# Kernel tuning notes

Measured on AMD Instinct MI355X. Metric: run time of the kernel, lower is better.

## Reference

```python
import jax, jax.numpy as jnp
import numpy as np

B, N, D = 8, 256, 64  # batch, n_entities, feature dim


def setup_inputs() -> dict:
    key = jax.random.key(0)
    ks = jax.random.split(key, 8)
    s = 0.02
    return {
        "emb1": jax.random.normal(ks[0], (B, N, D), jnp.float32),
        "emb2": jax.random.normal(ks[1], (B, N, N, D), jnp.float32),
        "W1a": jax.random.normal(ks[2], (3 * D, 128), jnp.float32) * s,
        "b1a": jnp.zeros((128,), jnp.float32),
        "W1b": jax.random.normal(ks[3], (128, D), jnp.float32) * s,
        "b1b": jnp.zeros((D,), jnp.float32),
        "W2a": jax.random.normal(ks[4], (4 * D, 256), jnp.float32) * s,
        "b2a": jnp.zeros((256,), jnp.float32),
        "W2b": jax.random.normal(ks[5], (256, D), jnp.float32) * s,
        "b2b": jnp.zeros((D,), jnp.float32),
    }


def _mlp(x, Wa, ba, Wb, bb):
    h = jax.nn.relu(jnp.einsum("...i,io->...o", x, Wa) + ba)
    return jnp.einsum("...i,io->...o", h, Wb) + bb


def reference(emb1, emb2, W1a, b1a, W1b, b1b, W2a, b2a, W2b, b2b):
    # arity 1: reduce arity-2 embedding over second entity dim (max & min), concat
    red_max = jnp.max(emb2, axis=-2)           # [B,N,D]
    red_min = jnp.min(emb2, axis=-2)           # [B,N,D]
    cat1 = jnp.concatenate([emb1, red_max, red_min], axis=-1)  # [B,N,3D]

    # arity 2: expand arity-1 embedding along a new entity dim, concat with emb2
    exp = jnp.broadcast_to(emb1[:, :, None, :], emb2.shape)    # [B,N,N,D]
    cat2 = jnp.concatenate([exp, emb2], axis=-1)               # [B,N,N,2D]

    # permutation gather: position (i,j) gets [cat2[j,i], cat2[i,j]] along features
    perm2 = jnp.concatenate([jnp.transpose(cat2, (0, 2, 1, 3)), cat2], axis=-1)  # [B,N,N,4D]

    out1 = _mlp(cat1, W1a, b1a, W1b, b1b)    # [B,N,D]
    out2 = _mlp(perm2, W2a, b2a, W2b, b2b)   # [B,N,N,D]
    return (out1, out2)
```

## Files before the change

### kernel.cpp

```cpp
#include <hip/hip_runtime.h>
#include <hip/hip_bf16.h>

typedef __bf16 bf16x8 __attribute__((ext_vector_type(8)));
typedef float f32x4 __attribute__((ext_vector_type(4)));
typedef unsigned int u32;
typedef unsigned short u16;
typedef u32 u32x4 __attribute__((ext_vector_type(4)));
typedef u16 u16x4 __attribute__((ext_vector_type(4)));

__device__ __forceinline__ u16 f2bf(float x) {
  u32 u = __float_as_uint(x);
  return (u16)((u + 0x7FFFu + ((u >> 16) & 1u)) >> 16);
}

__device__ __forceinline__ bf16x8 ld_frag_lds(const u16* base, int byteOff) {
  u32x4 v = *(const u32x4*)((const char*)base + byteOff);
  return __builtin_bit_cast(bf16x8, v);
}

__device__ __forceinline__ bf16x8 ld_frag_glb(const u16* p) {
  u32x4 v = *(const u32x4*)p;
  return __builtin_bit_cast(bf16x8, v);
}

__global__ void prep_kernel(const float* __restrict__ W2a, const float* __restrict__ W2b,
                            u16* __restrict__ wfA, u16* __restrict__ wfB) {
  int t = blockIdx.x * 256 + threadIdx.x;
  if (t < 8192) {
    int lane = t & 63;
    int ks = (t >> 6) & 7;
    int ntg = t >> 9;
    int col = (ntg << 4) + (lane & 15);
    int kb = (ks << 5) + ((lane >> 4) << 3);
#pragma unroll
    for (int q = 0; q < 8; ++q)
      wfA[t * 8 + q] = f2bf(W2a[(kb + q) * 256 + col]);
  } else if (t < 10240) {
    int t2 = t - 8192;
    int lane = t2 & 63;
    int ks = (t2 >> 6) & 7;
    int ntg = t2 >> 9;
    int col = (ntg << 4) + (lane & 15);
    int kb = (ks << 5) + ((lane >> 4) << 3);
#pragma unroll
    for (int q = 0; q < 8; ++q)
      wfB[t2 * 8 + q] = f2bf(W2b[(kb + q) * 64 + col]);
  }
}

__global__ __launch_bounds__(256) void out1_kernel(
    const float* __restrict__ emb1, const float* __restrict__ emb2,
    const float* __restrict__ W1a, const float* __restrict__ b1a,
    const float* __restrict__ W1b, const float* __restrict__ b1b,
    float* __restrict__ out1) {
  int bi = blockIdx.x;
  int t = threadIdx.x;
  __shared__ float smax[4][64];
  __shared__ float smin[4][64];
  __shared__ float cat1[192];
  __shared__ float h[128];

  int d = t & 63, q = t >> 6;
  const float* base = emb2 + (size_t)bi * 256 * 64;
  float vmax = -INFINITY, vmin = INFINITY;
  for (int j = q; j < 256; j += 4) {
    float v = base[j * 64 + d];
    vmax = fmaxf(vmax, v);
    vmin = fminf(vmin, v);
  }
  smax[q][d] = vmax;
  smin[q][d] = vmin;
  __syncthreads();
  if (t < 64) {
    float mx = fmaxf(fmaxf(smax[0][t], smax[1][t]), fmaxf(smax[2][t], smax[3][t]));
    float mn = fminf(fminf(smin[0][t], smin[1][t]), fminf(smin[2][t], smin[3][t]));
    cat1[t] = emb1[bi * 64 + t];
    cat1[64 + t] = mx;
    cat1[128 + t] = mn;
  }
  __syncthreads();
  if (t < 128) {
    float acc = b1a[t];
    for (int k = 0; k < 192; ++k) acc += cat1[k] * W1a[k * 128 + t];
    h[t] = fmaxf(acc, 0.f);
  }
  __syncthreads();
  if (t < 64) {
    float acc = b1b[t];
    for (int k = 0; k < 128; ++k) acc += h[k] * W1b[k * 64 + t];
    out1[bi * 64 + t] = acc;
  }
}

__global__ __launch_bounds__(256, 2) void out2_kernel(
    const float* __restrict__ emb1, const float* __restrict__ emb2,
    const float* __restrict__ b2a, const float* __restrict__ b2b,
    const u16* __restrict__ wfA, const u16* __restrict__ wfB,
    float* __restrict__ out2) {
  __shared__ __align__(16) u16 Xs[64 * 256];
  __shared__ __align__(16) u16 Hs[64 * 256];

  int blk = blockIdx.x;
  int b = blk >> 10;
  int i = (blk >> 2) & 255;
  int j0 = (blk & 3) << 6;
  int t = threadIdx.x;
  int lane = t & 63;
  int w = t >> 6;
  int lr = lane & 15;
  int lg = lane >> 4;

  {
    int r = t >> 2;
    int c0 = (t & 3) << 4;
    const float* s0 = emb1 + ((b << 8) + j0 + r) * 64;
    const float* s1 = emb2 + ((((size_t)(b << 8) + j0 + r) << 8) + i) * 64;
    const float* s2 = emb1 + ((b << 8) + i) * 64;
    const float* s3 = emb2 + ((((size_t)(b << 8) + i) << 8) + (j0 + r)) * 64;
    const float* srcs[4] = {s0, s1, s2, s3};
#pragma unroll
    for (int seg = 0; seg < 4; ++seg) {
      const float* src = srcs[seg];
#pragma unroll
      for (int u = 0; u < 4; ++u) {
        int d = c0 + (u << 2);
        float4 v = *(const float4*)(src + d);
        u16x4 o = {f2bf(v.x), f2bf(v.y), f2bf(v.z), f2bf(v.w)};
        int byteOff = (r * 512 + ((seg << 6) + d) * 2) ^ ((r & 7) << 4);
        *(u16x4*)((char*)Xs + byteOff) = o;
      }
    }
  }
  __syncthreads();

  f32x4 acc1[4][4];
#pragma unroll
  for (int m = 0; m < 4; ++m)
#pragma unroll
    for (int nt = 0; nt < 4; ++nt) acc1[m][nt] = (f32x4){0.f, 0.f, 0.f, 0.f};

#pragma unroll
  for (int ks = 0; ks < 8; ++ks) {
    int kByte = (ks << 6) + (lg << 4);
    bf16x8 a[4];
#pragma unroll
    for (int m = 0; m < 4; ++m) {
      int r = (m << 4) + lr;
      int off = (r * 512 + kByte) ^ ((r & 7) << 4);
      a[m] = ld_frag_lds(Xs, off);
    }
    bf16x8 bw[4];
#pragma unroll
    for (int nt = 0; nt < 4; ++nt)
      bw[nt] = ld_frag_glb(wfA + (size_t)((((w << 2) + nt) * 8 + ks) * 64 + lane) * 8);
#pragma unroll
    for (int m = 0; m < 4; ++m)
#pragma unroll
      for (int nt = 0; nt < 4; ++nt)
        acc1[m][nt] = __builtin_amdgcn_mfma_f32_16x16x32_bf16(a[m], bw[nt], acc1[m][nt], 0, 0, 0);
  }

#pragma unroll
  for (int nt = 0; nt < 4; ++nt) {
    int n = (w << 6) + (nt << 4) + lr;
    float bias = b2a[n];
#pragma unroll
    for (int m = 0; m < 4; ++m) {
      int r0 = (m << 4) + (lg << 2);
#pragma unroll
      for (int e = 0; e < 4; ++e) {
        int r = r0 + e;
        float hv = fmaxf(acc1[m][nt][e] + bias, 0.f);
        int off = (r * 512 + n * 2) ^ ((r & 7) << 4);
        *(u16*)((char*)Hs + off) = f2bf(hv);
      }
    }
  }
  __syncthreads();

  f32x4 acc2[4];
#pragma unroll
  for (int m = 0; m < 4; ++m) acc2[m] = (f32x4){0.f, 0.f, 0.f, 0.f};

#pragma unroll
  for (int ks = 0; ks < 8; ++ks) {
    int kByte = (ks << 6) + (lg << 4);
    bf16x8 bw = ld_frag_glb(wfB + (size_t)(((w << 3) + ks) * 64 + lane) * 8);
#pragma unroll
    for (int m = 0; m < 4; ++m) {
      int r = (m << 4) + lr;
      int off = (r * 512 + kByte) ^ ((r & 7) << 4);
      bf16x8 a = ld_frag_lds(Hs, off);
      acc2[m] = __builtin_amdgcn_mfma_f32_16x16x32_bf16(a, bw, acc2[m], 0, 0, 0);
    }
  }

  int col = (w << 4) + lr;
  float bias2 = b2b[col];
  float* obase = out2 + ((((size_t)(b << 8) + i) << 8) + j0) * 64;
#pragma unroll
  for (int m = 0; m < 4; ++m) {
    int r0 = (m << 4) + (lg << 2);
#pragma unroll
    for (int e = 0; e < 4; ++e)
      obase[(size_t)(r0 + e) * 64 + col] = acc2[m][e] + bias2;
  }
}

extern "C" void kernel_launch(void* const* d_in, const int* in_sizes, int n_in,
                              void* d_out, int out_size, void* d_ws, size_t ws_size,
                              hipStream_t stream) {
  const float* emb1 = (const float*)d_in[0];
  const float* emb2 = (const float*)d_in[1];
  const float* W1a  = (const float*)d_in[2];
  const float* b1a  = (const float*)d_in[3];
  const float* W1b  = (const float*)d_in[4];
  const float* b1b  = (const float*)d_in[5];
  const float* W2a  = (const float*)d_in[6];
  const float* b2a  = (const float*)d_in[7];
  const float* W2b  = (const float*)d_in[8];
  const float* b2b  = (const float*)d_in[9];

  float* out = (float*)d_out;
  u16* wfA = (u16*)d_ws;
  u16* wfB = wfA + 16 * 8 * 64 * 8;

  prep_kernel<<<40, 256, 0, stream>>>(W2a, W2b, wfA, wfB);
  out1_kernel<<<2048, 256, 0, stream>>>(emb1, emb2, W1a, b1a, W1b, b1b, out);
  out2_kernel<<<8192, 256, 0, stream>>>(emb1, emb2, b2a, b2b, wfA, wfB,
                                        out + 8 * 256 * 64);
}
```

Before: 162.8 us.

## Fuse out1 and out2 kernels and alias a single LDS buffer

Merges the out1 and out2 kernels into one launch: blocks at index 8192 and above do the arity-1 reduction and MLP, the rest do the arity-2 MFMA MLP. The separate X and H LDS buffers become one 32KB buffer reused after an extra barrier, so the LDS footprint per block is halved, and launch bounds rise to 5 blocks per SM. This is meant to cut launch overhead, let the small out1 work overlap with out2, and raise occupancy. The cost is one more __syncthreads and a tighter register budget that could cause spills.

```diff
diff --git a/kernel.cpp b/kernel.cpp
--- a/kernel.cpp
+++ b/kernel.cpp
@@ -48,63 +48,62 @@
   }
 }
 
-__global__ __launch_bounds__(256) void out1_kernel(
+__global__ __launch_bounds__(256, 5) void fused_kernel(
     const float* __restrict__ emb1, const float* __restrict__ emb2,
     const float* __restrict__ W1a, const float* __restrict__ b1a,
     const float* __restrict__ W1b, const float* __restrict__ b1b,
-    float* __restrict__ out1) {
-  int bi = blockIdx.x;
-  int t = threadIdx.x;
-  __shared__ float smax[4][64];
-  __shared__ float smin[4][64];
-  __shared__ float cat1[192];
-  __shared__ float h[128];
-
-  int d = t & 63, q = t >> 6;
-  const float* base = emb2 + (size_t)bi * 256 * 64;
-  float vmax = -INFINITY, vmin = INFINITY;
-  for (int j = q; j < 256; j += 4) {
-    float v = base[j * 64 + d];
-    vmax = fmaxf(vmax, v);
-    vmin = fminf(vmin, v);
-  }
-  smax[q][d] = vmax;
-  smin[q][d] = vmin;
-  __syncthreads();
-  if (t < 64) {
-    float mx = fmaxf(fmaxf(smax[0][t], smax[1][t]), fmaxf(smax[2][t], smax[3][t]));
-    float mn = fminf(fminf(smin[0][t], smin[1][t]), fminf(smin[2][t], smin[3][t]));
-    cat1[t] = emb1[bi * 64 + t];
-    cat1[64 + t] = mx;
-    cat1[128 + t] = mn;
-  }
-  __syncthreads();
-  if (t < 128) {
-    float acc = b1a[t];
-    for (int k = 0; k < 192; ++k) acc += cat1[k] * W1a[k * 128 + t];
-    h[t] = fmaxf(acc, 0.f);
-  }
-  __syncthreads();
-  if (t < 64) {
-    float acc = b1b[t];
-    for (int k = 0; k < 128; ++k) acc += h[k] * W1b[k * 64 + t];
-    out1[bi * 64 + t] = acc;
-  }
-}
-
-__global__ __launch_bounds__(256, 2) void out2_kernel(
-    const float* __restrict__ emb1, const float* __restrict__ emb2,
     const float* __restrict__ b2a, const float* __restrict__ b2b,
     const u16* __restrict__ wfA, const u16* __restrict__ wfB,
-    float* __restrict__ out2) {
-  __shared__ __align__(16) u16 Xs[64 * 256];
-  __shared__ __align__(16) u16 Hs[64 * 256];
+    float* __restrict__ out1, float* __restrict__ out2) {
+  __shared__ __align__(16) u16 S[64 * 256];
 
   int blk = blockIdx.x;
+  int t = threadIdx.x;
+
+  if (blk >= 8192) {
+    int bi = blk - 8192;
+    float* f = (float*)S;
+    float* smax = f;
+    float* smin = f + 256;
+    float* cat1 = f + 512;
+    float* h    = f + 704;
+
+    int d = t & 63, q = t >> 6;
+    const float* base = emb2 + (size_t)bi * 256 * 64;
+    float vmax = -INFINITY, vmin = INFINITY;
+    for (int j = q; j < 256; j += 4) {
+      float v = base[j * 64 + d];
+      vmax = fmaxf(vmax, v);
+      vmin = fminf(vmin, v);
+    }
+    smax[q * 64 + d] = vmax;
+    smin[q * 64 + d] = vmin;
+    __syncthreads();
+    if (t < 64) {
+      float mx = fmaxf(fmaxf(smax[t], smax[64 + t]), fmaxf(smax[128 + t], smax[192 + t]));
+      float mn = fminf(fminf(smin[t], smin[64 + t]), fminf(smin[128 + t], smin[192 + t]));
+      cat1[t] = emb1[bi * 64 + t];
+      cat1[64 + t] = mx;
+      cat1[128 + t] = mn;
+    }
+    __syncthreads();
+    if (t < 128) {
+      float acc = b1a[t];
+      for (int k = 0; k < 192; ++k) acc += cat1[k] * W1a[k * 128 + t];
+      h[t] = fmaxf(acc, 0.f);
+    }
+    __syncthreads();
+    if (t < 64) {
+      float acc = b1b[t];
+      for (int k = 0; k < 128; ++k) acc += h[k] * W1b[k * 64 + t];
+      out1[bi * 64 + t] = acc;
+    }
+    return;
+  }
+
   int b = blk >> 10;
   int i = (blk >> 2) & 255;
   int j0 = (blk & 3) << 6;
-  int t = threadIdx.x;
   int lane = t & 63;
   int w = t >> 6;
   int lr = lane & 15;
@@ -127,7 +126,7 @@
         float4 v = *(const float4*)(src + d);
         u16x4 o = {f2bf(v.x), f2bf(v.y), f2bf(v.z), f2bf(v.w)};
         int byteOff = (r * 512 + ((seg << 6) + d) * 2) ^ ((r & 7) << 4);
-        *(u16x4*)((char*)Xs + byteOff) = o;
+        *(u16x4*)((char*)S + byteOff) = o;
       }
     }
   }
@@ -147,7 +146,7 @@
     for (int m = 0; m < 4; ++m) {
       int r = (m << 4) + lr;
       int off = (r * 512 + kByte) ^ ((r & 7) << 4);
-      a[m] = ld_frag_lds(Xs, off);
+      a[m] = ld_frag_lds(S, off);
     }
     bf16x8 bw[4];
 #pragma unroll
@@ -159,6 +158,8 @@
       for (int nt = 0; nt < 4; ++nt)
         acc1[m][nt] = __builtin_amdgcn_mfma_f32_16x16x32_bf16(a[m], bw[nt], acc1[m][nt], 0, 0, 0);
   }
+
+  __syncthreads();
 
 #pragma unroll
   for (int nt = 0; nt < 4; ++nt) {
@@ -172,7 +173,7 @@
         int r = r0 + e;
         float hv = fmaxf(acc1[m][nt][e] + bias, 0.f);
         int off = (r * 512 + n * 2) ^ ((r & 7) << 4);
-        *(u16*)((char*)Hs + off) = f2bf(hv);
+        *(u16*)((char*)S + off) = f2bf(hv);
       }
     }
   }
@@ -190,7 +191,7 @@
     for (int m = 0; m < 4; ++m) {
       int r = (m << 4) + lr;
       int off = (r * 512 + kByte) ^ ((r & 7) << 4);
-      bf16x8 a = ld_frag_lds(Hs, off);
+      bf16x8 a = ld_frag_lds(S, off);
       acc2[m] = __builtin_amdgcn_mfma_f32_16x16x32_bf16(a, bw, acc2[m], 0, 0, 0);
     }
   }
@@ -226,7 +227,7 @@
   u16* wfB = wfA + 16 * 8 * 64 * 8;
 
   prep_kernel<<<40, 256, 0, stream>>>(W2a, W2b, wfA, wfB);
-  out1_kernel<<<2048, 256, 0, stream>>>(emb1, emb2, W1a, b1a, W1b, b1b, out);
-  out2_kernel<<<8192, 256, 0, stream>>>(emb1, emb2, b2a, b2b, wfA, wfB,
-                                        out + 8 * 256 * 64);
-}
+  fused_kernel<<<10240, 256, 0, stream>>>(emb1, emb2, W1a, b1a, W1b, b1b,
+                                          b2a, b2b, wfA, wfB,
+                                          out, out + 8 * 256 * 64);
+}
```

Result: slower. 485.2 us (+198.0%).

## Precompute emb1[i] projection, shrink K to 192, double-buffer j tiles per block

Applied to the files above, without the earlier changes.

The emb1[i] segment of the first layer's input is constant across j for a given (b,i), so its product with W2a (plus bias) is precomputed once per row in a new prep kernel. The main GEMM's K drops from 256 to 192. Each block now covers all 256 j for one (b,i) in four 64-row tiles. Staging of the next tile is overlapped with compute through LDS double buffering, and the W2b fragments are held in registers across tiles. The MFMA operands are swapped so H and the output are written as vectors. This cuts redundant FLOPs and global loads, at the cost of an extra kernel launch, more registers, and fewer, longer blocks.

```diff
diff --git a/kernel.cpp b/kernel.cpp
--- a/kernel.cpp
+++ b/kernel.cpp
@@ -7,45 +7,64 @@
 typedef unsigned short u16;
 typedef u32 u32x4 __attribute__((ext_vector_type(4)));
 typedef u16 u16x4 __attribute__((ext_vector_type(4)));
+typedef u16 u16x8 __attribute__((ext_vector_type(8)));
 
 __device__ __forceinline__ u16 f2bf(float x) {
   u32 u = __float_as_uint(x);
   return (u16)((u + 0x7FFFu + ((u >> 16) & 1u)) >> 16);
 }
+__device__ __forceinline__ u16 cvt_bf16(float x) {
+  __bf16 h = (__bf16)x;
+  return __builtin_bit_cast(u16, h);
+}
 
 __device__ __forceinline__ bf16x8 ld_frag_lds(const u16* base, int byteOff) {
   u32x4 v = *(const u32x4*)((const char*)base + byteOff);
   return __builtin_bit_cast(bf16x8, v);
 }
-
 __device__ __forceinline__ bf16x8 ld_frag_glb(const u16* p) {
   u32x4 v = *(const u32x4*)p;
   return __builtin_bit_cast(bf16x8, v);
 }
 
-__global__ void prep_kernel(const float* __restrict__ W2a, const float* __restrict__ W2b,
-                            u16* __restrict__ wfA, u16* __restrict__ wfB) {
+__global__ void prep_w_kernel(const float* __restrict__ W2a, const float* __restrict__ W2b,
+                              u16* __restrict__ wfA, u16* __restrict__ wfB) {
   int t = blockIdx.x * 256 + threadIdx.x;
-  if (t < 8192) {
+  if (t < 6144) {
     int lane = t & 63;
-    int ks = (t >> 6) & 7;
-    int ntg = t >> 9;
+    int ks = (t >> 6) % 6;
+    int ntg = t / 384;
     int col = (ntg << 4) + (lane & 15);
-    int kb = (ks << 5) + ((lane >> 4) << 3);
+    int kk = (ks << 5) + ((lane >> 4) << 3);
+    int row = kk + (kk >= 128 ? 64 : 0);
 #pragma unroll
     for (int q = 0; q < 8; ++q)
-      wfA[t * 8 + q] = f2bf(W2a[(kb + q) * 256 + col]);
-  } else if (t < 10240) {
-    int t2 = t - 8192;
+      wfA[t * 8 + q] = f2bf(W2a[(row + q) * 256 + col]);
+  } else if (t < 8192) {
+    int t2 = t - 6144;
     int lane = t2 & 63;
     int ks = (t2 >> 6) & 7;
     int ntg = t2 >> 9;
     int col = (ntg << 4) + (lane & 15);
-    int kb = (ks << 5) + ((lane >> 4) << 3);
+    int k = (ks << 5) + ((lane >> 4) << 3);
 #pragma unroll
     for (int q = 0; q < 8; ++q)
-      wfB[t2 * 8 + q] = f2bf(W2b[(kb + q) * 64 + col]);
-  }
+      wfB[t2 * 8 + q] = f2bf(W2b[(k + q) * 64 + col]);
+  }
+}
+
+__global__ __launch_bounds__(256) void prep_T2_kernel(
+    const float* __restrict__ emb1, const float* __restrict__ W2a,
+    const float* __restrict__ b2a, float* __restrict__ T2p) {
+  __shared__ float e1row[64];
+  int bn = blockIdx.x;
+  int t = threadIdx.x;
+  if (t < 64) e1row[t] = emb1[bn * 64 + t];
+  __syncthreads();
+  float a = b2a[t];
+#pragma unroll 8
+  for (int k = 0; k < 64; ++k) a += e1row[k] * W2a[(128 + k) * 256 + t];
+  T2p[(size_t)bn * 256 + t] = a;
 }
 
 __global__ __launch_bounds__(256) void out1_kernel(
@@ -94,116 +113,153 @@
 
 __global__ __launch_bounds__(256, 2) void out2_kernel(
     const float* __restrict__ emb1, const float* __restrict__ emb2,
-    const float* __restrict__ b2a, const float* __restrict__ b2b,
+    const float* __restrict__ b2b,
     const u16* __restrict__ wfA, const u16* __restrict__ wfB,
-    float* __restrict__ out2) {
-  __shared__ __align__(16) u16 Xs[64 * 256];
-  __shared__ __align__(16) u16 Hs[64 * 256];
+    const float* __restrict__ T2p, float* __restrict__ out2) {
+  __shared__ __align__(16) u16 SH[40960];
 
   int blk = blockIdx.x;
-  int b = blk >> 10;
-  int i = (blk >> 2) & 255;
-  int j0 = (blk & 3) << 6;
+  int b = blk >> 8;
+  int i = blk & 255;
   int t = threadIdx.x;
   int lane = t & 63;
   int w = t >> 6;
   int lr = lane & 15;
   int lg = lane >> 4;
 
-  {
-    int r = t >> 2;
-    int c0 = (t & 3) << 4;
-    const float* s0 = emb1 + ((b << 8) + j0 + r) * 64;
-    const float* s1 = emb2 + ((((size_t)(b << 8) + j0 + r) << 8) + i) * 64;
-    const float* s2 = emb1 + ((b << 8) + i) * 64;
-    const float* s3 = emb2 + ((((size_t)(b << 8) + i) << 8) + (j0 + r)) * 64;
-    const float* srcs[4] = {s0, s1, s2, s3};
-#pragma unroll
-    for (int seg = 0; seg < 4; ++seg) {
-      const float* src = srcs[seg];
-#pragma unroll
-      for (int u = 0; u < 4; ++u) {
-        int d = c0 + (u << 2);
-        float4 v = *(const float4*)(src + d);
-        u16x4 o = {f2bf(v.x), f2bf(v.y), f2bf(v.z), f2bf(v.w)};
-        int byteOff = (r * 512 + ((seg << 6) + d) * 2) ^ ((r & 7) << 4);
-        *(u16x4*)((char*)Xs + byteOff) = o;
+  u16* X0 = SH;
+  u16* X1 = SH + 12288;
+  u16* H = SH + 24576;
+  char* Hb = (char*)SH + 49152;
+
+  bf16x8 wb[8];
+#pragma unroll
+  for (int ks = 0; ks < 8; ++ks)
+    wb[ks] = ld_frag_glb(wfB + (size_t)(((w << 3) + ks) * 64 + lane) * 8);
+  float4 t2v[4];
+#pragma unroll
+  for (int nt = 0; nt < 4; ++nt)
+    t2v[nt] = *(const float4*)(T2p + ((size_t)(b << 8) + i) * 256 +
+                               (w << 6) + (nt << 4) + (lg << 2));
+  float4 bias2 = *(const float4*)(b2b + (w << 4) + (lg << 2));
+  float* oblk = out2 + (((size_t)(b << 8) + i) << 8) * 64 + (w << 4) + (lg << 2);
+
+  int sr = t >> 2, sq = t & 3;
+  float4 vs[12];
+
+  auto stage_load = [&](int j0n) {
+    const float* s0 = emb1 + (((b << 8) + j0n + sr) << 6);
+    const float* s1 = emb2 + (((size_t)((b << 8) + j0n + sr) << 8) + i) * 64;
+    const float* s2 = emb2 + (((size_t)((b << 8) + i) << 8) + (j0n + sr)) * 64;
+#pragma unroll
+    for (int ch = 0; ch < 3; ++ch) {
+      int c = sq * 48 + ch * 16;
+      int seg = c >> 6, off = c & 63;
+      const float* src = (seg == 0 ? s0 : (seg == 1 ? s1 : s2)) + off;
+#pragma unroll
+      for (int u = 0; u < 4; ++u) vs[ch * 4 + u] = *(const float4*)(src + (u << 2));
+    }
+  };
+  auto stage_write = [&](u16* Xn) {
+    char* Xb = (char*)Xn;
+    int swz = (sr & 7) << 4;
+#pragma unroll
+    for (int ch = 0; ch < 3; ++ch) {
+      int cb = (sq * 48 + ch * 16) * 2;
+      float4 a0 = vs[ch * 4 + 0], a1 = vs[ch * 4 + 1];
+      float4 a2 = vs[ch * 4 + 2], a3 = vs[ch * 4 + 3];
+      u16x8 o0 = {cvt_bf16(a0.x), cvt_bf16(a0.y), cvt_bf16(a0.z), cvt_bf16(a0.w),
+                  cvt_bf16(a1.x), cvt_bf16(a1.y), cvt_bf16(a1.z), cvt_bf16(a1.w)};
+      u16x8 o1 = {cvt_bf16(a2.x), cvt_bf16(a2.y), cvt_bf16(a2.z), cvt_bf16(a2.w),
+                  cvt_bf16(a3.x), cvt_bf16(a3.y), cvt_bf16(a3.z), cvt_bf16(a3.w)};
+      *(u16x8*)(Xb + ((sr * 384 + cb) ^ swz)) = o0;
+      *(u16x8*)(Xb + ((sr * 384 + cb + 16) ^ swz)) = o1;
+    }
+  };
+
+  stage_load(0);
+  stage_write(X0);
+  __syncthreads();
+
+#pragma unroll
+  for (int g = 0; g < 4; ++g) {
+    int j0 = g << 6;
+    u16* Xc = (g & 1) ? X1 : X0;
+    u16* Xn = (g & 1) ? X0 : X1;
+
+    if (g < 3) stage_load(j0 + 64);
+
+    f32x4 acc1[4][4];
+#pragma unroll
+    for (int m = 0; m < 4; ++m)
+#pragma unroll
+      for (int nt = 0; nt < 4; ++nt) acc1[m][nt] = (f32x4){0.f, 0.f, 0.f, 0.f};
+
+#pragma unroll
+    for (int ks = 0; ks < 6; ++ks) {
+      int kByte = (ks << 6) + (lg << 4);
+      bf16x8 a[4];
+#pragma unroll
+      for (int m = 0; m < 4; ++m) {
+        int row = (m << 4) + lr;
+        a[m] = ld_frag_lds(Xc, (row * 384 + kByte) ^ ((lr & 7) << 4));
       }
-    }
-  }
-  __syncthreads();
-
-  f32x4 acc1[4][4];
-#pragma unroll
-  for (int m = 0; m < 4; ++m)
-#pragma unroll
-    for (int nt = 0; nt < 4; ++nt) acc1[m][nt] = (f32x4){0.f, 0.f, 0.f, 0.f};
-
-#pragma unroll
-  for (int ks = 0; ks < 8; ++ks) {
-    int kByte = (ks << 6) + (lg << 4);
-    bf16x8 a[4];
-#pragma unroll
-    for (int m = 0; m < 4; ++m) {
-      int r = (m << 4) + lr;
-      int off = (r * 512 + kByte) ^ ((r & 7) << 4);
-      a[m] = ld_frag_lds(Xs, off);
-    }
-    bf16x8 bw[4];
-#pragma unroll
-    for (int nt = 0; nt < 4; ++nt)
-      bw[nt] = ld_frag_glb(wfA + (size_t)((((w << 2) + nt) * 8 + ks) * 64 + lane) * 8);
-#pragma unroll
-    for (int m = 0; m < 4; ++m)
+      bf16x8 bw[4];
 #pragma unroll
       for (int nt = 0; nt < 4; ++nt)
-        acc1[m][nt] = __builtin_amdgcn_mfma_f32_16x16x32_bf16(a[m], bw[nt], acc1[m][nt], 0, 0, 0);
-  }
-
-#pragma unroll
-  for (int nt = 0; nt < 4; ++nt) {
-    int n = (w << 6) + (nt << 4) + lr;
-    float bias = b2a[n];
-#pragma unroll
-    for (int m = 0; m < 4; ++m) {
-      int r0 = (m << 4) + (lg << 2);
-#pragma unroll
-      for (int e = 0; e < 4; ++e) {
-        int r = r0 + e;
-        float hv = fmaxf(acc1[m][nt][e] + bias, 0.f);
-        int off = (r * 512 + n * 2) ^ ((r & 7) << 4);
-        *(u16*)((char*)Hs + off) = f2bf(hv);
+        bw[nt] = ld_frag_glb(wfA + (size_t)((((w << 2) + nt) * 6 + ks) * 64 + lane) * 8);
+#pragma unroll
+      for (int m = 0; m < 4; ++m)
+#pragma unroll
+        for (int nt = 0; nt < 4; ++nt)
+          acc1[m][nt] = __builtin_amdgcn_mfma_f32_16x16x32_bf16(bw[nt], a[m], acc1[m][nt], 0, 0, 0);
+    }
+
+#pragma unroll
+    for (int nt = 0; nt < 4; ++nt) {
+      int n_lo = (((w << 2) + nt) << 4) + (lg << 2);
+#pragma unroll
+      for (int m = 0; m < 4; ++m) {
+        int jrow = (m << 4) + lr;
+        u16x4 o = {cvt_bf16(fmaxf(acc1[m][nt][0] + t2v[nt].x, 0.f)),
+                   cvt_bf16(fmaxf(acc1[m][nt][1] + t2v[nt].y, 0.f)),
+                   cvt_bf16(fmaxf(acc1[m][nt][2] + t2v[nt].z, 0.f)),
+                   cvt_bf16(fmaxf(acc1[m][nt][3] + t2v[nt].w, 0.f))};
+        *(u16x4*)(Hb + ((jrow * 512 + n_lo * 2) ^ ((lr & 7) << 4))) = o;
       }
     }
-  }
-  __syncthreads();
-
-  f32x4 acc2[4];
-#pragma unroll
-  for (int m = 0; m < 4; ++m) acc2[m] = (f32x4){0.f, 0.f, 0.f, 0.f};
-
-#pragma unroll
-  for (int ks = 0; ks < 8; ++ks) {
-    int kByte = (ks << 6) + (lg << 4);
-    bf16x8 bw = ld_frag_glb(wfB + (size_t)(((w << 3) + ks) * 64 + lane) * 8);
-#pragma unroll
-    for (int m = 0; m < 4; ++m) {
-      int r = (m << 4) + lr;
-      int off = (r * 512 + kByte) ^ ((r & 7) << 4);
-      bf16x8 a = ld_frag_lds(Hs, off);
-      acc2[m] = __builtin_amdgcn_mfma_f32_16x16x32_bf16(a, bw, acc2[m], 0, 0, 0);
-    }
-  }
-
-  int col = (w << 4) + lr;
-  float bias2 = b2b[col];
-  float* obase = out2 + ((((size_t)(b << 8) + i) << 8) + j0) * 64;
-#pragma unroll
-  for (int m = 0; m < 4; ++m) {
-    int r0 = (m << 4) + (lg << 2);
-#pragma unroll
-    for (int e = 0; e < 4; ++e)
-      obase[(size_t)(r0 + e) * 64 + col] = acc2[m][e] + bias2;
+
+    if (g < 3) stage_write(Xn);
+
+    asm volatile("s_waitcnt lgkmcnt(0)");
+    __builtin_amdgcn_s_barrier();
+    __builtin_amdgcn_sched_barrier(0);
+
+    f32x4 acc2[4];
+#pragma unroll
+    for (int jt = 0; jt < 4; ++jt) acc2[jt] = (f32x4){0.f, 0.f, 0.f, 0.f};
+
+#pragma unroll
+    for (int ks = 0; ks < 8; ++ks) {
+      int kByte = (ks << 6) + (lg << 4);
+#pragma unroll
+      for (int jt = 0; jt < 4; ++jt) {
+        int row = (jt << 4) + lr;
+        bf16x8 hfr = ld_frag_lds(H, (row * 512 + kByte) ^ ((lr & 7) << 4));
+        acc2[jt] = __builtin_amdgcn_mfma_f32_16x16x32_bf16(wb[ks], hfr, acc2[jt], 0, 0, 0);
+      }
+    }
+
+    float* obase = oblk + (size_t)j0 * 64;
+#pragma unroll
+    for (int jt = 0; jt < 4; ++jt) {
+      float4 v = {acc2[jt][0] + bias2.x, acc2[jt][1] + bias2.y,
+                  acc2[jt][2] + bias2.z, acc2[jt][3] + bias2.w};
+      *(float4*)(obase + (size_t)((jt << 4) + lr) * 64) = v;
+    }
+
+    __builtin_amdgcn_s_barrier();
+    __builtin_amdgcn_sched_barrier(0);
   }
 }
 
@@ -223,10 +279,12 @@
 
   float* out = (float*)d_out;
   u16* wfA = (u16*)d_ws;
-  u16* wfB = wfA + 16 * 8 * 64 * 8;
-
-  prep_kernel<<<40, 256, 0, stream>>>(W2a, W2b, wfA, wfB);
+  u16* wfB = wfA + 49152;
+  float* T2p = (float*)(wfB + 16384);
+
+  prep_w_kernel<<<32, 256, 0, stream>>>(W2a, W2b, wfA, wfB);
+  prep_T2_kernel<<<2048, 256, 0, stream>>>(emb1, W2a, b2a, T2p);
   out1_kernel<<<2048, 256, 0, stream>>>(emb1, emb2, W1a, b1a, W1b, b1b, out);
-  out2_kernel<<<8192, 256, 0, stream>>>(emb1, emb2, b2a, b2b, wfA, wfB,
+  out2_kernel<<<2048, 256, 0, stream>>>(emb1, emb2, b2b, wfA, wfB, T2p,
                                         out + 8 * 256 * 64);
 }
```

Measured after the change: 259.0 us (median of 4 runs). +59.1%, slower.

## Keep hidden activations in registers and split second GEMM by K with LDS reduction

Applied to the files above, without the earlier changes.

The first GEMM now uses swapped MFMA operands, so each lane holds hidden-unit values in the layout the second GEMM expects as its B operand. ReLU outputs are packed to bf16 in registers and fed straight into the second MFMA, with no round trip through LDS. Each wave computes a K-slice of all 64 output columns, and the partial sums are then reduced across waves through LDS. The weight prep is reordered to match, LDS is merged into one 48KB buffer, staging stores are widened to 16 bytes, and output stores use float4. The cost is more accumulator registers and an extra cross-wave reduction pass.

```diff
diff --git a/kernel.cpp b/kernel.cpp
--- a/kernel.cpp
+++ b/kernel.cpp
@@ -7,24 +7,28 @@
 typedef unsigned short u16;
 typedef u32 u32x4 __attribute__((ext_vector_type(4)));
 typedef u16 u16x4 __attribute__((ext_vector_type(4)));
+typedef u16 u16x8 __attribute__((ext_vector_type(8)));
 
 __device__ __forceinline__ u16 f2bf(float x) {
   u32 u = __float_as_uint(x);
   return (u16)((u + 0x7FFFu + ((u >> 16) & 1u)) >> 16);
 }
+__device__ __forceinline__ u16 cvt_bf16(float x) {
+  __bf16 h = (__bf16)x;
+  return __builtin_bit_cast(u16, h);
+}
 
 __device__ __forceinline__ bf16x8 ld_frag_lds(const u16* base, int byteOff) {
   u32x4 v = *(const u32x4*)((const char*)base + byteOff);
   return __builtin_bit_cast(bf16x8, v);
 }
-
 __device__ __forceinline__ bf16x8 ld_frag_glb(const u16* p) {
   u32x4 v = *(const u32x4*)p;
   return __builtin_bit_cast(bf16x8, v);
 }
 
-__global__ void prep_kernel(const float* __restrict__ W2a, const float* __restrict__ W2b,
-                            u16* __restrict__ wfA, u16* __restrict__ wfB) {
+__global__ void prep_w_kernel(const float* __restrict__ W2a, const float* __restrict__ W2b,
+                              u16* __restrict__ wfA, u16* __restrict__ wfB2) {
   int t = blockIdx.x * 256 + threadIdx.x;
   if (t < 8192) {
     int lane = t & 63;
@@ -36,15 +40,19 @@
     for (int q = 0; q < 8; ++q)
       wfA[t * 8 + q] = f2bf(W2a[(kb + q) * 256 + col]);
   } else if (t < 10240) {
-    int t2 = t - 8192;
-    int lane = t2 & 63;
-    int ks = (t2 >> 6) & 7;
-    int ntg = t2 >> 9;
-    int col = (ntg << 4) + (lane & 15);
-    int kb = (ks << 5) + ((lane >> 4) << 3);
-#pragma unroll
-    for (int q = 0; q < 8; ++q)
-      wfB[t2 * 8 + q] = f2bf(W2b[(kb + q) * 64 + col]);
+    int t2i = t - 8192;
+    int lane = t2i & 63;
+    int dt = (t2i >> 6) & 3;
+    int tt = (t2i >> 8) & 1;
+    int w = t2i >> 9;
+    int g = lane >> 4, c = lane & 15;
+    int col = (dt << 4) + c;
+#pragma unroll
+    for (int q = 0; q < 8; ++q) {
+      int pi = (q < 4) ? (g * 4 + q) : (16 + g * 4 + (q - 4));
+      int n = w * 64 + tt * 32 + pi;
+      wfB2[t2i * 8 + q] = f2bf(W2b[n * 64 + col]);
+    }
   }
 }
 
@@ -95,10 +103,9 @@
 __global__ __launch_bounds__(256, 2) void out2_kernel(
     const float* __restrict__ emb1, const float* __restrict__ emb2,
     const float* __restrict__ b2a, const float* __restrict__ b2b,
-    const u16* __restrict__ wfA, const u16* __restrict__ wfB,
+    const u16* __restrict__ wfA, const u16* __restrict__ wfB2,
     float* __restrict__ out2) {
-  __shared__ __align__(16) u16 Xs[64 * 256];
-  __shared__ __align__(16) u16 Hs[64 * 256];
+  __shared__ __align__(16) u16 SH[24576];
 
   int blk = blockIdx.x;
   int b = blk >> 10;
@@ -112,7 +119,7 @@
 
   {
     int r = t >> 2;
-    int c0 = (t & 3) << 4;
+    int c16 = (t & 3) << 4;
     const float* s0 = emb1 + ((b << 8) + j0 + r) * 64;
     const float* s1 = emb2 + ((((size_t)(b << 8) + j0 + r) << 8) + i) * 64;
     const float* s2 = emb1 + ((b << 8) + i) * 64;
@@ -122,12 +129,14 @@
     for (int seg = 0; seg < 4; ++seg) {
       const float* src = srcs[seg];
 #pragma unroll
-      for (int u = 0; u < 4; ++u) {
-        int d = c0 + (u << 2);
-        float4 v = *(const float4*)(src + d);
-        u16x4 o = {f2bf(v.x), f2bf(v.y), f2bf(v.z), f2bf(v.w)};
+      for (int u = 0; u < 2; ++u) {
+        int d = c16 + (u << 3);
+        float4 v0 = *(const float4*)(src + d);
+        float4 v1 = *(const float4*)(src + d + 4);
+        u16x8 o = {cvt_bf16(v0.x), cvt_bf16(v0.y), cvt_bf16(v0.z), cvt_bf16(v0.w),
+                   cvt_bf16(v1.x), cvt_bf16(v1.y), cvt_bf16(v1.z), cvt_bf16(v1.w)};
         int byteOff = (r * 512 + ((seg << 6) + d) * 2) ^ ((r & 7) << 4);
-        *(u16x4*)((char*)Xs + byteOff) = o;
+        *(u16x8*)((char*)SH + byteOff) = o;
       }
     }
   }
@@ -145,9 +154,8 @@
     bf16x8 a[4];
 #pragma unroll
     for (int m = 0; m < 4; ++m) {
-      int r = (m << 4) + lr;
-      int off = (r * 512 + kByte) ^ ((r & 7) << 4);
-      a[m] = ld_frag_lds(Xs, off);
+      int row = (m << 4) + lr;
+      a[m] = ld_frag_lds(SH, (row * 512 + kByte) ^ ((lr & 7) << 4));
     }
     bf16x8 bw[4];
 #pragma unroll
@@ -157,53 +165,81 @@
     for (int m = 0; m < 4; ++m)
 #pragma unroll
       for (int nt = 0; nt < 4; ++nt)
-        acc1[m][nt] = __builtin_amdgcn_mfma_f32_16x16x32_bf16(a[m], bw[nt], acc1[m][nt], 0, 0, 0);
-  }
-
-#pragma unroll
-  for (int nt = 0; nt < 4; ++nt) {
-    int n = (w << 6) + (nt << 4) + lr;
-    float bias = b2a[n];
+        acc1[m][nt] = __builtin_amdgcn_mfma_f32_16x16x32_bf16(bw[nt], a[m], acc1[m][nt], 0, 0, 0);
+  }
+
+  __syncthreads();
+
+  f32x4 acc2[4][4];
+#pragma unroll
+  for (int m = 0; m < 4; ++m)
+#pragma unroll
+    for (int dt = 0; dt < 4; ++dt) acc2[m][dt] = (f32x4){0.f, 0.f, 0.f, 0.f};
+
+#pragma unroll
+  for (int t2 = 0; t2 < 2; ++t2) {
+    int nbase = (w << 6) + (t2 << 5) + (lg << 2);
+    float4 ba = *(const float4*)(b2a + nbase);
+    float4 bb = *(const float4*)(b2a + nbase + 16);
+    bf16x8 h[4];
 #pragma unroll
     for (int m = 0; m < 4; ++m) {
-      int r0 = (m << 4) + (lg << 2);
-#pragma unroll
-      for (int e = 0; e < 4; ++e) {
-        int r = r0 + e;
-        float hv = fmaxf(acc1[m][nt][e] + bias, 0.f);
-        int off = (r * 512 + n * 2) ^ ((r & 7) << 4);
-        *(u16*)((char*)Hs + off) = f2bf(hv);
+      f32x4 pa = acc1[m][2 * t2];
+      f32x4 pb = acc1[m][2 * t2 + 1];
+      u16x8 hp = {cvt_bf16(fmaxf(pa[0] + ba.x, 0.f)), cvt_bf16(fmaxf(pa[1] + ba.y, 0.f)),
+                  cvt_bf16(fmaxf(pa[2] + ba.z, 0.f)), cvt_bf16(fmaxf(pa[3] + ba.w, 0.f)),
+                  cvt_bf16(fmaxf(pb[0] + bb.x, 0.f)), cvt_bf16(fmaxf(pb[1] + bb.y, 0.f)),
+                  cvt_bf16(fmaxf(pb[2] + bb.z, 0.f)), cvt_bf16(fmaxf(pb[3] + bb.w, 0.f))};
+      h[m] = __builtin_bit_cast(bf16x8, hp);
+    }
+#pragma unroll
+    for (int dt = 0; dt < 4; ++dt) {
+      bf16x8 wf = ld_frag_glb(wfB2 + (size_t)(((((w << 1) + t2) << 2) + dt) * 64 + lane) * 8);
+#pragma unroll
+      for (int m = 0; m < 4; ++m)
+        acc2[m][dt] = __builtin_amdgcn_mfma_f32_16x16x32_bf16(wf, h[m], acc2[m][dt], 0, 0, 0);
+    }
+  }
+
+  char* red = (char*)SH;
+#pragma unroll
+  for (int dt = 0; dt < 4; ++dt) {
+    if (dt != w) {
+      int s = dt - (dt > w ? 1 : 0);
+#pragma unroll
+      for (int m = 0; m < 4; ++m)
+        *(f32x4*)(red + ((((w * 3 + s) << 2) + m) << 10) + (lane << 4)) = acc2[m][dt];
+    }
+  }
+  __syncthreads();
+
+  f32x4 accO[4];
+#pragma unroll
+  for (int m = 0; m < 4; ++m) {
+    accO[m] = acc2[m][0];
+#pragma unroll
+    for (int dt = 1; dt < 4; ++dt)
+      if (w == dt) accO[m] = acc2[m][dt];
+  }
+#pragma unroll
+  for (int wp = 0; wp < 4; ++wp) {
+    if (wp != w) {
+      int s = w - (w > wp ? 1 : 0);
+#pragma unroll
+      for (int m = 0; m < 4; ++m) {
+        f32x4 p = *(const f32x4*)(red + ((((wp * 3 + s) << 2) + m) << 10) + (lane << 4));
+        accO[m] += p;
       }
     }
   }
-  __syncthreads();
-
-  f32x4 acc2[4];
-#pragma unroll
-  for (int m = 0; m < 4; ++m) acc2[m] = (f32x4){0.f, 0.f, 0.f, 0.f};
-
-#pragma unroll
-  for (int ks = 0; ks < 8; ++ks) {
-    int kByte = (ks << 6) + (lg << 4);
-    bf16x8 bw = ld_frag_glb(wfB + (size_t)(((w << 3) + ks) * 64 + lane) * 8);
-#pragma unroll
-    for (int m = 0; m < 4; ++m) {
-      int r = (m << 4) + lr;
-      int off = (r * 512 + kByte) ^ ((r & 7) << 4);
-      bf16x8 a = ld_frag_lds(Hs, off);
-      acc2[m] = __builtin_amdgcn_mfma_f32_16x16x32_bf16(a, bw, acc2[m], 0, 0, 0);
-    }
-  }
-
-  int col = (w << 4) + lr;
-  float bias2 = b2b[col];
-  float* obase = out2 + ((((size_t)(b << 8) + i) << 8) + j0) * 64;
+
+  float4 bias2 = *(const float4*)(b2b + (w << 4) + (lg << 2));
+  float* obase = out2 + (((size_t)(b << 8) + i) * 256 + j0) * 64 + (w << 4) + (lg << 2);
 #pragma unroll
   for (int m = 0; m < 4; ++m) {
-    int r0 = (m << 4) + (lg << 2);
-#pragma unroll
-    for (int e = 0; e < 4; ++e)
-      obase[(size_t)(r0 + e) * 64 + col] = acc2[m][e] + bias2;
+    float4 v = {accO[m][0] + bias2.x, accO[m][1] + bias2.y,
+                accO[m][2] + bias2.z, accO[m][3] + bias2.w};
+    *(float4*)(obase + (size_t)((m << 4) + lr) * 64) = v;
   }
 }
 
@@ -222,11 +258,11 @@
   const float* b2b  = (const float*)d_in[9];
 
   float* out = (float*)d_out;
-  u16* wfA = (u16*)d_ws;
-  u16* wfB = wfA + 16 * 8 * 64 * 8;
-
-  prep_kernel<<<40, 256, 0, stream>>>(W2a, W2b, wfA, wfB);
+  u16* wfA  = (u16*)d_ws;
+  u16* wfB2 = wfA + 65536;
+
+  prep_w_kernel<<<40, 256, 0, stream>>>(W2a, W2b, wfA, wfB2);
   out1_kernel<<<2048, 256, 0, stream>>>(emb1, emb2, W1a, b1a, W1b, b1b, out);
-  out2_kernel<<<8192, 256, 0, stream>>>(emb1, emb2, b2a, b2b, wfA, wfB,
+  out2_kernel<<<8192, 256, 0, stream>>>(emb1, emb2, b2a, b2b, wfA, wfB2,
                                         out + 8 * 256 * 64);
 }
```

After: 152.6 us. -6.3%, faster.
